# Optimization experiments

Hardware: AMD Instinct MI355X
Metric: run time of the kernel (lower is better)

## Reference

```python
import jax, jax.numpy as jnp
import numpy as np

NUM_LAYERS = 20   # num_layers init arg
RPRIME = 1.0      # Rprime init arg
HIDDEN = 512      # hidden_size
G, P = 64, 16     # num polygons, polygon size (graph.structure)
N, D = 65536, 2   # points, input_size


def _simplex_project(x):
    """KDS.activate: sort-based Euclidean projection onto the probability simplex, rows of x."""
    n = x.shape[-1]
    u = -jnp.sort(-x, axis=-1)                                   # descending sort
    v = (jnp.cumsum(u, axis=-1) - 1.0) / jnp.arange(1, n + 1, dtype=x.dtype)
    k = jnp.sum(u > v, axis=-1) - 1                               # rho - 1 (always >= 0)
    w = jnp.take_along_axis(v, k[..., None], axis=-1)             # threshold tau per row
    return jax.nn.relu(x - w)


def _nesterov_coeff(layer):
    return layer / (layer + 3.0)


def _poca(y, A, step):
    """point_of_closest_approach: accelerated projected GD onto conv hull of A's rows.
    y: [N, D], A: [P, D] -> [N, D]"""
    n = y.shape[0]
    p = A.shape[0]
    init = (jnp.zeros((n, p), y.dtype), jnp.zeros((n, p), y.dtype))  # (x_tmp, x_old)

    def body(carry, layer):
        x_tmp, x_old = carry
        Q = jnp.nan_to_num(y - x_tmp @ A)          # [N, D]
        grad = -(Q @ A.T)                          # [N, P]
        x_new = _simplex_project(x_tmp - grad * step)
        x_tmp_next = x_new + _nesterov_coeff(layer) * (x_new - x_old)
        return (x_tmp_next, x_new), None

    (_, x_new), _ = jax.lax.scan(body, init, jnp.arange(NUM_LAYERS, dtype=y.dtype))
    return x_new @ A                               # [N, D]


def setup_inputs() -> dict:
    key = jax.random.key(0)
    k1, k2, k3, k4 = jax.random.split(key, 4)
    y = jax.random.normal(k1, (N, D), dtype=jnp.float32)
    W = jax.random.normal(k2, (HIDDEN, D), dtype=jnp.float32)
    step = jax.random.uniform(k3, (1,), dtype=jnp.float32)
    polygons = jax.random.randint(k4, (G, P), 0, HIDDEN, dtype=jnp.int32)
    return {"y": y, "W": W, "step": step, "polygons": polygons}


def reference(y, W, step, polygons):
    """KDS.forward with accelerate=True == encode_accelerated(y).
    Returns (yhat, f, f0) matching the torch module's encode output."""
    step_s = step[0]
    A = W[polygons]                                               # [G, P, D] gather
    points = jax.vmap(lambda a: _poca(y, a, step_s))(A)           # [G, N, D]

    # gradient is constant across outer iterations: [N, G+1]
    dist = jnp.sqrt(jnp.sum((y[None, :, :] - points) ** 2, axis=-1) / (RPRIME ** 2))  # [G, N]
    grad = jnp.concatenate([jnp.ones((y.shape[0], 1), y.dtype), dist.T], axis=1)

    init = (jnp.zeros((y.shape[0], G + 1), y.dtype),
            jnp.zeros((y.shape[0], G + 1), y.dtype))              # (f_tmp, f_old)

    def body(carry, layer):
        f_tmp, f_old = carry
        f_new = _simplex_project(f_tmp - grad * step_s)
        f_tmp_next = f_new + _nesterov_coeff(layer) * (f_new - f_old)
        return (f_tmp_next, f_new), None

    (_, f_new), _ = jax.lax.scan(body, init, jnp.arange(NUM_LAYERS, dtype=y.dtype))

    yhat = y * f_new[:, :1] + jnp.einsum('ng,gnd->nd', f_new[:, 1:], points)
    return yhat, f_new[:, 1:], f_new[:, 0]
```

## Files before the change

### kernel.cpp

```cpp
#include <hip/hip_runtime.h>
#include <math.h>

#define NPTS  65536
#define NG    64
#define NP    16
#define NLAY  20

struct Net { int a[63]; int b[63]; int cnt; };
constexpr Net make_batcher16() {
    Net net{};
    int c = 0;
    const int n = 16;
    for (int p = 1; p < n; p <<= 1)
        for (int k = p; k >= 1; k >>= 1)
            for (int j = k % p; j + k < n; j += 2 * k)
                for (int i = 0; i < k && i + j + k < n; ++i)
                    if ((i + j) / (2 * p) == (i + j + k) / (2 * p)) {
                        net.a[c] = i + j;
                        net.b[c] = i + j + k;
                        ++c;
                    }
    net.cnt = c;
    return net;
}
constexpr Net BNET = make_batcher16();
static_assert(BNET.cnt == 63, "Batcher-16 must have exactly 63 comparators");
constexpr bool stage1_is_disjoint_pairs() {
    for (int c = 0; c < 8; ++c)
        if (BNET.a[c] != 2 * c || BNET.b[c] != 2 * c + 1) return false;
    return true;
}
static_assert(stage1_is_disjoint_pairs(), "stage-1 copy-absorption invalid");

__device__ __forceinline__ float simplex_tau(const float* __restrict__ x,
                                             float* __restrict__ u) {
#pragma unroll
    for (int c = 0; c < 8; ++c) {
        const int ia = BNET.a[c], ib = BNET.b[c];
        u[ia] = fmaxf(x[ia], x[ib]);
        u[ib] = fminf(x[ia], x[ib]);
    }
#pragma unroll
    for (int c = 8; c < 63; ++c) {
        const int ia = BNET.a[c], ib = BNET.b[c];
        const float mx = fmaxf(u[ia], u[ib]);
        const float mn = fminf(u[ia], u[ib]);
        u[ia] = mx; u[ib] = mn;
    }
    float vv[NP];
    float cs = u[0];
    vv[0] = cs - 1.0f;
#pragma unroll
    for (int j = 1; j < NP; ++j) {
        cs += u[j];
        const float r = 1.0f / (float)(j + 1);
        vv[j] = fmaf(cs, r, -r);
    }
    float m0 = fmaxf(fmaxf(vv[0], vv[1]), vv[2]);
    float m1 = fmaxf(fmaxf(vv[3], vv[4]), vv[5]);
    float m2 = fmaxf(fmaxf(vv[6], vv[7]), vv[8]);
    float m3 = fmaxf(fmaxf(vv[9], vv[10]), vv[11]);
    float m4 = fmaxf(fmaxf(vv[12], vv[13]), vv[14]);
    float m5 = vv[15];
    float n0 = fmaxf(fmaxf(m0, m1), m2);
    float n1 = fmaxf(fmaxf(m3, m4), m5);
    return fmaxf(n0, n1);
}

__global__ __launch_bounds__(256) void poca_kernel(
    const float2* __restrict__ y2, const float* __restrict__ W,
    const float* __restrict__ step_p, const int* __restrict__ polys,
    float2* __restrict__ pts)
{
    const int g = blockIdx.y;
    const int n = blockIdx.x * 256 + threadIdx.x;
    const float step = step_p[0];
    const float rs = sqrtf(step);
    const float inv_rs = 1.0f / rs;

    float a0[NP], a1[NP];
#pragma unroll
    for (int p = 0; p < NP; ++p) {
        const int idx = polys[g * NP + p];
        a0[p] = rs * W[idx * 2 + 0];
        a1[p] = rs * W[idx * 2 + 1];
    }

    const float2 yv = y2[n];
    const float y0 = rs * yv.x;
    const float y1 = rs * yv.y;

    float xt[NP], xo[NP], x[NP], u[NP];

#pragma unroll
    for (int p = 0; p < NP; ++p)
        x[p] = fmaf(y0, a0[p], y1 * a1[p]);
    {
        const float tau = simplex_tau(x, u);
#pragma unroll
        for (int p = 0; p < NP; ++p) {
            const float xn = fmaxf(x[p] - tau, 0.f);
            xt[p] = xn; xo[p] = xn;
        }
    }

    for (int layer = 1; layer < NLAY; ++layer) {
        float q0 = y0, q1 = y1;
#pragma unroll
        for (int p = 0; p < NP; ++p) {
            q0 = fmaf(-xt[p], a0[p], q0);
            q1 = fmaf(-xt[p], a1[p], q1);
        }
#pragma unroll
        for (int p = 0; p < NP; ++p)
            x[p] = fmaf(q0, a0[p], fmaf(q1, a1[p], xt[p]));

        const float tau = simplex_tau(x, u);

        const float cn = (float)layer / ((float)layer + 3.0f);
#pragma unroll
        for (int p = 0; p < NP; ++p) {
            const float xn = fmaxf(x[p] - tau, 0.f);
            xt[p] = fmaf(cn, xn - xo[p], xn);
            xo[p] = xn;
        }
    }

    float p0 = 0.f, p1 = 0.f;
#pragma unroll
    for (int p = 0; p < NP; ++p) {
        p0 = fmaf(xo[p], a0[p], p0);
        p1 = fmaf(xo[p], a1[p], p1);
    }
    pts[(size_t)g * NPTS + n] = make_float2(p0 * inv_rs, p1 * inv_rs);
}

__global__ __launch_bounds__(256) void fiter_kernel(
    const float* __restrict__ y, const float* __restrict__ step_p,
    const float2* __restrict__ pts, float* __restrict__ out)
{
    const int n = blockIdx.x * 256 + threadIdx.x;
    const float step = step_p[0];
    const float y0 = y[2 * n + 0];
    const float y1 = y[2 * n + 1];

    float gs[NG + 1];
    gs[0] = step;
#pragma unroll
    for (int g = 0; g < NG; ++g) {
        const float2 p = pts[(size_t)g * NPTS + n];
        const float dx = y0 - p.x;
        const float dy = y1 - p.y;
        gs[1 + g] = sqrtf(dx * dx + dy * dy) * step;
    }

    float x[NG + 1], fo[NG + 1];
#pragma unroll
    for (int i = 0; i <= NG; ++i) { x[i] = 0.f; fo[i] = 0.f; }

    for (int layer = 0; layer < NLAY; ++layer) {
        float s0 = 0.f, s1 = 0.f, s2 = 0.f, s3 = 0.f;
#pragma unroll
        for (int i = 0; i <= NG; ++i) {
            x[i] -= gs[i];
            if ((i & 3) == 0)      s0 += x[i];
            else if ((i & 3) == 1) s1 += x[i];
            else if ((i & 3) == 2) s2 += x[i];
            else                   s3 += x[i];
        }
        float tau = ((s0 + s1) + (s2 + s3) - 1.0f) * (1.0f / 65.0f);
        int kprev = NG + 1;
        for (int pass = 0; pass < NG + 1; ++pass) {
            float t0 = 0.f, t1 = 0.f, t2 = 0.f, t3 = 0.f;
            int cnt = 0;
#pragma unroll
            for (int i = 0; i <= NG; ++i) {
                const bool in = x[i] > tau;
                const float xv = in ? x[i] : 0.f;
                if ((i & 3) == 0)      t0 += xv;
                else if ((i & 3) == 1) t1 += xv;
                else if ((i & 3) == 2) t2 += xv;
                else                   t3 += xv;
                cnt += in ? 1 : 0;
            }
            if (cnt == kprev) break;
            kprev = cnt;
            tau = (((t0 + t1) + (t2 + t3)) - 1.0f) / (float)cnt;
        }
        const float c = (float)layer / ((float)layer + 3.0f);
#pragma unroll
        for (int i = 0; i <= NG; ++i) {
            const float fn = fmaxf(x[i] - tau, 0.f);
            x[i] = fmaf(c, fn - fo[i], fn);
            fo[i] = fn;
        }
    }

    float acc0 = y0 * fo[0];
    float acc1 = y1 * fo[0];
#pragma unroll
    for (int g = 0; g < NG; ++g) {
        const float2 p = pts[(size_t)g * NPTS + n];
        acc0 = fmaf(fo[1 + g], p.x, acc0);
        acc1 = fmaf(fo[1 + g], p.y, acc1);
    }

    ((float2*)out)[n] = make_float2(acc0, acc1);
    float4* fsec = (float4*)(out + 2 * (size_t)NPTS);
#pragma unroll
    for (int g4 = 0; g4 < NG / 4; ++g4) {
        fsec[(size_t)n * (NG / 4) + g4] = make_float4(
            fo[1 + 4 * g4], fo[2 + 4 * g4], fo[3 + 4 * g4], fo[4 + 4 * g4]);
    }
    out[2 * (size_t)NPTS + (size_t)NPTS * NG + n] = fo[0];
}

extern "C" void kernel_launch(void* const* d_in, const int* in_sizes, int n_in,
                              void* d_out, int out_size, void* d_ws, size_t ws_size,
                              hipStream_t stream) {
    const float*  y     = (const float*)d_in[0];
    const float2* y2    = (const float2*)d_in[0];
    const float*  W     = (const float*)d_in[1];
    const float*  step  = (const float*)d_in[2];
    const int*    polys = (const int*)d_in[3];
    float*        out   = (float*)d_out;
    float2*       pts   = (float2*)d_ws;

    dim3 gridA(NPTS / 256, NG);
    poca_kernel<<<gridA, 256, 0, stream>>>(y2, W, step, polys, pts);
    fiter_kernel<<<NPTS / 256, 256, 0, stream>>>(y, step, pts, out);
}
```

Measured before the change: 677.4 us.

## Split fiter simplex iteration across four lanes per point with shuffle reductions

The second kernel now assigns four threads to each point, each holding 16 of the 64 polygon weights, while the bias column lives only on the lead lane (other lanes hold a large negative sentinel). Sums, counts and the final weighted accumulation are combined with xor shuffles. This cuts per-thread register arrays from 65 to 16 elements and launches four times as many threads, aiming to improve occupancy and parallelism in the fixed-point simplex projection. The cost is extra shuffles in every pass of the iterative threshold loop, and a divergent early-exit check, though all four lanes see the same reduced values.

Result: faster. 638.0 us (-5.8%).

```diff
diff --git a/kernel.cpp b/kernel.cpp
--- a/kernel.cpp
+++ b/kernel.cpp
@@ -136,89 +136,119 @@
 }
 
 __global__ __launch_bounds__(256) void fiter_kernel(
-    const float* __restrict__ y, const float* __restrict__ step_p,
+    const float2* __restrict__ y2, const float* __restrict__ step_p,
     const float2* __restrict__ pts, float* __restrict__ out)
 {
-    const int n = blockIdx.x * 256 + threadIdx.x;
+    const int gt = blockIdx.x * 256 + threadIdx.x;
+    const int n  = gt >> 2;
+    const int s  = gt & 3;
+    const bool lead = (s == 0);
+    const float NEG = -1e30f;
     const float step = step_p[0];
-    const float y0 = y[2 * n + 0];
-    const float y1 = y[2 * n + 1];
-
-    float gs[NG + 1];
-    gs[0] = step;
-#pragma unroll
-    for (int g = 0; g < NG; ++g) {
-        const float2 p = pts[(size_t)g * NPTS + n];
+    const float2 yv = y2[n];
+    const float y0 = yv.x, y1 = yv.y;
+
+    float gs[16];
+#pragma unroll
+    for (int j = 0; j < 16; ++j) {
+        const float2 p = pts[(size_t)(16 * s + j) * NPTS + n];
         const float dx = y0 - p.x;
         const float dy = y1 - p.y;
-        gs[1 + g] = sqrtf(dx * dx + dy * dy) * step;
-    }
-
-    float x[NG + 1], fo[NG + 1];
-#pragma unroll
-    for (int i = 0; i <= NG; ++i) { x[i] = 0.f; fo[i] = 0.f; }
+        gs[j] = sqrtf(dx * dx + dy * dy) * step;
+    }
+    const float gs0 = lead ? step : 0.f;
+    const float msk0 = lead ? 1.f : 0.f;
+
+    float x[16], fo[16];
+#pragma unroll
+    for (int j = 0; j < 16; ++j) { x[j] = 0.f; fo[j] = 0.f; }
+    float x0 = lead ? 0.f : NEG;
+    float fo0 = 0.f;
 
     for (int layer = 0; layer < NLAY; ++layer) {
-        float s0 = 0.f, s1 = 0.f, s2 = 0.f, s3 = 0.f;
-#pragma unroll
-        for (int i = 0; i <= NG; ++i) {
-            x[i] -= gs[i];
-            if ((i & 3) == 0)      s0 += x[i];
-            else if ((i & 3) == 1) s1 += x[i];
-            else if ((i & 3) == 2) s2 += x[i];
-            else                   s3 += x[i];
-        }
-        float tau = ((s0 + s1) + (s2 + s3) - 1.0f) * (1.0f / 65.0f);
-        int kprev = NG + 1;
+        float t0 = 0.f, t1 = 0.f, t2 = 0.f, t3 = 0.f;
+#pragma unroll
+        for (int j = 0; j < 16; ++j) {
+            x[j] -= gs[j];
+            if ((j & 3) == 0)      t0 += x[j];
+            else if ((j & 3) == 1) t1 += x[j];
+            else if ((j & 3) == 2) t2 += x[j];
+            else                   t3 += x[j];
+        }
+        x0 -= gs0;
+        float t = (t0 + t1) + (t2 + t3);
+        t = fmaf(msk0, x0, t);
+        t += __shfl_xor(t, 1);
+        t += __shfl_xor(t, 2);
+        float tau = (t - 1.0f) * (1.0f / 65.0f);
+
+        float kprev = 65.f;
         for (int pass = 0; pass < NG + 1; ++pass) {
-            float t0 = 0.f, t1 = 0.f, t2 = 0.f, t3 = 0.f;
-            int cnt = 0;
-#pragma unroll
-            for (int i = 0; i <= NG; ++i) {
-                const bool in = x[i] > tau;
-                const float xv = in ? x[i] : 0.f;
-                if ((i & 3) == 0)      t0 += xv;
-                else if ((i & 3) == 1) t1 += xv;
-                else if ((i & 3) == 2) t2 += xv;
-                else                   t3 += xv;
-                cnt += in ? 1 : 0;
+            float a0 = 0.f, a1 = 0.f, a2 = 0.f, a3 = 0.f;
+            float c0 = 0.f, c1 = 0.f, c2 = 0.f, c3 = 0.f;
+#pragma unroll
+            for (int j = 0; j < 16; ++j) {
+                const float f = (x[j] > tau) ? 1.f : 0.f;
+                if ((j & 3) == 0)      { a0 = fmaf(f, x[j], a0); c0 += f; }
+                else if ((j & 3) == 1) { a1 = fmaf(f, x[j], a1); c1 += f; }
+                else if ((j & 3) == 2) { a2 = fmaf(f, x[j], a2); c2 += f; }
+                else                   { a3 = fmaf(f, x[j], a3); c3 += f; }
             }
-            if (cnt == kprev) break;
-            kprev = cnt;
-            tau = (((t0 + t1) + (t2 + t3)) - 1.0f) / (float)cnt;
-        }
+            const float f0 = (x0 > tau) ? 1.f : 0.f;
+            float aa = (a0 + a1) + (a2 + a3);
+            aa = fmaf(f0, x0, aa);
+            float cc = ((c0 + c1) + (c2 + c3)) + f0;
+            aa += __shfl_xor(aa, 1);
+            aa += __shfl_xor(aa, 2);
+            cc += __shfl_xor(cc, 1);
+            cc += __shfl_xor(cc, 2);
+            if (cc == kprev) break;
+            kprev = cc;
+            tau = (aa - 1.0f) / cc;
+        }
+
         const float c = (float)layer / ((float)layer + 3.0f);
 #pragma unroll
-        for (int i = 0; i <= NG; ++i) {
-            const float fn = fmaxf(x[i] - tau, 0.f);
-            x[i] = fmaf(c, fn - fo[i], fn);
-            fo[i] = fn;
-        }
-    }
-
-    float acc0 = y0 * fo[0];
-    float acc1 = y1 * fo[0];
-#pragma unroll
-    for (int g = 0; g < NG; ++g) {
-        const float2 p = pts[(size_t)g * NPTS + n];
-        acc0 = fmaf(fo[1 + g], p.x, acc0);
-        acc1 = fmaf(fo[1 + g], p.y, acc1);
-    }
-
-    ((float2*)out)[n] = make_float2(acc0, acc1);
+        for (int j = 0; j < 16; ++j) {
+            const float fn = fmaxf(x[j] - tau, 0.f);
+            x[j] = fmaf(c, fn - fo[j], fn);
+            fo[j] = fn;
+        }
+        const float fn0 = fmaxf(x0 - tau, 0.f);
+        const float xt0 = fmaf(c, fn0 - fo0, fn0);
+        fo0 = fn0;
+        x0 = lead ? xt0 : NEG;
+    }
+
+    float acc0 = 0.f, acc1 = 0.f;
+#pragma unroll
+    for (int j = 0; j < 16; ++j) {
+        const float2 p = pts[(size_t)(16 * s + j) * NPTS + n];
+        acc0 = fmaf(fo[j], p.x, acc0);
+        acc1 = fmaf(fo[j], p.y, acc1);
+    }
+    acc0 += __shfl_xor(acc0, 1);
+    acc0 += __shfl_xor(acc0, 2);
+    acc1 += __shfl_xor(acc1, 1);
+    acc1 += __shfl_xor(acc1, 2);
+
     float4* fsec = (float4*)(out + 2 * (size_t)NPTS);
 #pragma unroll
-    for (int g4 = 0; g4 < NG / 4; ++g4) {
-        fsec[(size_t)n * (NG / 4) + g4] = make_float4(
-            fo[1 + 4 * g4], fo[2 + 4 * g4], fo[3 + 4 * g4], fo[4 + 4 * g4]);
-    }
-    out[2 * (size_t)NPTS + (size_t)NPTS * NG + n] = fo[0];
+    for (int q = 0; q < 4; ++q) {
+        fsec[(size_t)n * 16 + 4 * s + q] = make_float4(
+            fo[4 * q + 0], fo[4 * q + 1], fo[4 * q + 2], fo[4 * q + 3]);
+    }
+
+    if (lead) {
+        ((float2*)out)[n] = make_float2(fmaf(y0, fo0, acc0),
+                                        fmaf(y1, fo0, acc1));
+        out[2 * (size_t)NPTS + (size_t)NPTS * NG + n] = fo0;
+    }
 }
 
 extern "C" void kernel_launch(void* const* d_in, const int* in_sizes, int n_in,
                               void* d_out, int out_size, void* d_ws, size_t ws_size,
                               hipStream_t stream) {
-    const float*  y     = (const float*)d_in[0];
     const float2* y2    = (const float2*)d_in[0];
     const float*  W     = (const float*)d_in[1];
     const float*  step  = (const float*)d_in[2];
@@ -228,5 +258,5 @@
 
     dim3 gridA(NPTS / 256, NG);
     poca_kernel<<<gridA, 256, 0, stream>>>(y2, W, step, polys, pts);
-    fiter_kernel<<<NPTS / 256, 256, 0, stream>>>(y, step, pts, out);
-}
+    fiter_kernel<<<NPTS * 4 / 256, 256, 0, stream>>>(y2, step, pts, out);
+}
```
